# Performance work log

Measured on AMD Instinct MI355X. Metric: run time of the kernel, lower is better.

Reference implementation:

```python
import jax, jax.numpy as jnp
import numpy as np

N, M, D, H, T = 8192, 8192, 64, 32, 8
KERNEL_SCALE = 1.0


def setup_inputs() -> dict:
    key = jax.random.key(0)
    ks = jax.random.split(key, 8)
    s1 = 1.0 / np.sqrt(D)
    s2 = 1.0 / np.sqrt(H)
    return {
        "X": jax.random.normal(ks[0], (N, D), jnp.float32),
        "Y": jax.random.normal(ks[1], (M, D), jnp.float32),
        "Y_target": jax.random.normal(ks[2], (M, T), jnp.float32),
        "W1": jax.random.normal(ks[3], (D, H), jnp.float32) * s1,
        "b1": jnp.zeros((H,), jnp.float32),
        "W2": jax.random.normal(ks[4], (H, H), jnp.float32) * s2,
        "b2": jnp.zeros((H,), jnp.float32),
        "W3": jax.random.normal(ks[5], (H, H), jnp.float32) * s2,
        "b3": jnp.zeros((H,), jnp.float32),
    }


def _mlp(x, W1, b1, W2, b2, W3, b3):
    h = jax.nn.relu(x @ W1 + b1)
    h = jax.nn.relu(h @ W2 + b2)
    return jax.nn.relu(h @ W3 + b3)


def reference(X, Y, Y_target, W1, b1, W2, b2, W3, b3):
    Xf = _mlp(X, W1, b1, W2, b2, W3, b3)  # [N, H]
    Yf = _mlp(Y, W1, b1, W2, b2, W3, b3)  # [M, H]
    sq = (
        jnp.sum(Xf * Xf, axis=1, keepdims=True)
        + jnp.sum(Yf * Yf, axis=1)[None, :]
        - 2.0 * (Xf @ Yf.T)
    )
    sq = jnp.maximum(sq, 0.0)  # guard tiny negatives from cancellation
    kernel = jnp.exp(-sq / (2.0 * KERNEL_SCALE**2))  # [N, M]
    weights = kernel / jnp.sum(kernel, axis=1, keepdims=True)
    return weights @ Y_target  # [N, T]
```

## Files before the change

kernel.cpp:

```cpp
#include <hip/hip_runtime.h>
#include <hip/hip_bf16.h>
#include <cstddef>

#define N_ROWS 8192
#define M_ROWS 8192
#define D_IN   64
#define H_DIM  32
#define T_OUT  8
#define FDIM   48

#define NSPLIT   32
#define JSLICE   (M_ROWS / NSPLIT)
#define JTILE    32
#define NTILES   (JSLICE / JTILE)
#define LOG2E    1.4426950408889634f
#define NHALF_SC (-0.72134752044448169f)

#define KH_OFF 0
#define KL_OFF 3072
#define YH_OFF 6144
#define YL_OFF 8192
#define BUFSZ  10240
#define STAGESZ (2 * BUFSZ)

typedef _Float16 half8  __attribute__((ext_vector_type(8)));
typedef _Float16 half4v __attribute__((ext_vector_type(4)));
typedef __fp16   fp16x2 __attribute__((ext_vector_type(2)));
typedef float    f32x16 __attribute__((ext_vector_type(16)));

__device__ __forceinline__ half8 ld_h8(const _Float16* p) {
    return *(const half8*)p;
}


__global__ __launch_bounds__(256) void prep_kernel(
    const float* __restrict__ X, const float* __restrict__ Y,
    const float* __restrict__ Yt,
    const float* __restrict__ W1, const float* __restrict__ b1,
    const float* __restrict__ W2, const float* __restrict__ b2,
    const float* __restrict__ W3, const float* __restrict__ b3,
    _Float16* __restrict__ fh, _Float16* __restrict__ fl,
    _Float16* __restrict__ yfh, _Float16* __restrict__ yfl)
{
    __shared__ float xs [32 * 65];
    __shared__ float w1l[64 * 36];
    __shared__ float w2l[32 * 36];
    __shared__ float w3l[32 * 36];
    __shared__ float h1t[32 * 33];
    __shared__ float h2t[32 * 33];
    __shared__ float psums[8 * 32];
    __shared__ float bl[96];

    const int tid = threadIdx.x;

    if (blockIdx.x >= 512) {
        const int idx = (blockIdx.x - 512) * 256 + tid;
        const int lane = idx & 63;
        const int jtg  = idx >> 6;
        const int g    = jtg & 3;
        const int jt   = jtg >> 2;
        const int t    = lane & 31;
        const int h    = lane >> 5;
        const int j    = jt * 32 + g * 8 + h * 4;
        union { _Float16 hh[4]; uint2 u; } H, L;
        #pragma unroll
        for (int i = 0; i < 4; ++i) {
            float v = (t < T_OUT) ? Yt[(size_t)(j + i) * T_OUT + t]
                                  : (t == 8 ? 1.0f : 0.0f);
            _Float16 hi = (_Float16)v;
            H.hh[i] = hi;
            L.hh[i] = (_Float16)(v - (float)hi);
        }
        *(uint2*)(yfh + (size_t)idx * 4) = H.u;
        *(uint2*)(yfl + (size_t)idx * 4) = L.u;
        return;
    }

    const int rowbase = blockIdx.x * 32;
    const bool isX = rowbase < N_ROWS;
    const float* src = isX ? (X + (size_t)rowbase * D_IN)
                           : (Y + (size_t)(rowbase - N_ROWS) * D_IN);

    {
        const float4* g4 = (const float4*)src;
        int i0 = tid * 2;
        float4 v0 = g4[i0], v1 = g4[i0 + 1];
        int f0 = tid * 8;
        int r = f0 >> 6, c = f0 & 63;
        float* dst = xs + r * 65 + c;
        dst[0] = v0.x; dst[1] = v0.y; dst[2] = v0.z; dst[3] = v0.w;
        dst[4] = v1.x; dst[5] = v1.y; dst[6] = v1.z; dst[7] = v1.w;
    }
    {
        const float4* g4 = (const float4*)W1;
        int i0 = tid * 2;
        float4 v0 = g4[i0], v1 = g4[i0 + 1];
        int f0 = tid * 8;
        int r = f0 >> 5, c = f0 & 31;
        float* dst = w1l + r * 36 + c;
        ((float4*)dst)[0] = v0; ((float4*)dst)[1] = v1;
    }
    {
        int f0 = tid * 4;
        int r = f0 >> 5, c = f0 & 31;
        *(float4*)(w2l + r * 36 + c) = ((const float4*)W2)[tid];
        *(float4*)(w3l + r * 36 + c) = ((const float4*)W3)[tid];
    }
    if (tid < 32) { bl[tid] = b1[tid]; bl[32 + tid] = b2[tid]; bl[64 + tid] = b3[tid]; }
    __syncthreads();

    const int r  = tid & 31;
    const int c0 = (tid >> 5) * 4;

    float4 a1 = *(const float4*)(bl + c0);
    #pragma unroll
    for (int k = 0; k < 64; ++k) {
        float xv = xs[r * 65 + k];
        float4 w = *(const float4*)(w1l + k * 36 + c0);
        a1.x = fmaf(xv, w.x, a1.x);
        a1.y = fmaf(xv, w.y, a1.y);
        a1.z = fmaf(xv, w.z, a1.z);
        a1.w = fmaf(xv, w.w, a1.w);
    }
    h1t[(c0 + 0) * 33 + r] = fmaxf(a1.x, 0.f);
    h1t[(c0 + 1) * 33 + r] = fmaxf(a1.y, 0.f);
    h1t[(c0 + 2) * 33 + r] = fmaxf(a1.z, 0.f);
    h1t[(c0 + 3) * 33 + r] = fmaxf(a1.w, 0.f);
    __syncthreads();

    float4 a2 = *(const float4*)(bl + 32 + c0);
    #pragma unroll
    for (int k = 0; k < 32; ++k) {
        float xv = h1t[k * 33 + r];
        float4 w = *(const float4*)(w2l + k * 36 + c0);
        a2.x = fmaf(xv, w.x, a2.x);
        a2.y = fmaf(xv, w.y, a2.y);
        a2.z = fmaf(xv, w.z, a2.z);
        a2.w = fmaf(xv, w.w, a2.w);
    }
    h2t[(c0 + 0) * 33 + r] = fmaxf(a2.x, 0.f);
    h2t[(c0 + 1) * 33 + r] = fmaxf(a2.y, 0.f);
    h2t[(c0 + 2) * 33 + r] = fmaxf(a2.z, 0.f);
    h2t[(c0 + 3) * 33 + r] = fmaxf(a2.w, 0.f);
    __syncthreads();

    float4 a3 = *(const float4*)(bl + 64 + c0);
    #pragma unroll
    for (int k = 0; k < 32; ++k) {
        float xv = h2t[k * 33 + r];
        float4 w = *(const float4*)(w3l + k * 36 + c0);
        a3.x = fmaf(xv, w.x, a3.x);
        a3.y = fmaf(xv, w.y, a3.y);
        a3.z = fmaf(xv, w.z, a3.z);
        a3.w = fmaf(xv, w.w, a3.w);
    }
    float v0 = fmaxf(a3.x, 0.f), v1 = fmaxf(a3.y, 0.f);
    float v2 = fmaxf(a3.z, 0.f), v3 = fmaxf(a3.w, 0.f);

    psums[(tid >> 5) * 32 + r] = v0 * v0 + v1 * v1 + v2 * v2 + v3 * v3;

    const float scale = isX ? LOG2E : 1.0f;
    union { _Float16 h[4]; uint2 u; } hh, ll;
    float sv0 = v0 * scale, sv1 = v1 * scale, sv2 = v2 * scale, sv3 = v3 * scale;
    hh.h[0] = (_Float16)sv0; hh.h[1] = (_Float16)sv1;
    hh.h[2] = (_Float16)sv2; hh.h[3] = (_Float16)sv3;
    ll.h[0] = (_Float16)(sv0 - (float)hh.h[0]);
    ll.h[1] = (_Float16)(sv1 - (float)hh.h[1]);
    ll.h[2] = (_Float16)(sv2 - (float)hh.h[2]);
    ll.h[3] = (_Float16)(sv3 - (float)hh.h[3]);
    {
        const int tile = blockIdx.x;
        const int ch = c0 >> 4, hb = (c0 >> 3) & 1, off = c0 & 7;
        const size_t fi = (((size_t)(tile * 3 + ch) * 64) + hb * 32 + r) * 8 + off;
        *(uint2*)(fh + fi) = hh.u;
        *(uint2*)(fl + fi) = ll.u;
    }

    __syncthreads();
    if (tid < 32) {
        float nrm = 0.f;
        #pragma unroll
        for (int g = 0; g < 8; ++g) nrm += psums[g * 32 + tid];
        float qn = NHALF_SC * nrm;
        float d32 = isX ? qn : 1.0f;
        float d33 = isX ? 1.0f : qn;
        union { _Float16 h[8]; uint4 q; } eh, el, ez;
        #pragma unroll
        for (int i = 0; i < 8; ++i) { eh.h[i] = (_Float16)0.f; el.h[i] = (_Float16)0.f; ez.h[i] = (_Float16)0.f; }
        _Float16 h32 = (_Float16)d32, h33 = (_Float16)d33;
        eh.h[0] = h32; eh.h[1] = h33;
        el.h[0] = (_Float16)(d32 - (float)h32);
        el.h[1] = (_Float16)(d33 - (float)h33);
        const int tile = blockIdx.x;
        const size_t f0 = (((size_t)(tile * 3 + 2) * 64) + tid) * 8;
        const size_t f1 = (((size_t)(tile * 3 + 2) * 64) + 32 + tid) * 8;
        *(uint4*)(fh + f0) = eh.q;  *(uint4*)(fh + f1) = ez.q;
        *(uint4*)(fl + f0) = el.q;  *(uint4*)(fl + f1) = ez.q;
    }
}

__global__ __launch_bounds__(256, 4) void pair_kernel(
    const _Float16* __restrict__ fh, const _Float16* __restrict__ fl,
    const _Float16* __restrict__ yfh, const _Float16* __restrict__ yfl,
    float* __restrict__ pout, float* __restrict__ psum)
{
    __shared__ char smem[2 * STAGESZ];

    const int tid  = threadIdx.x;
    const int wave = tid >> 6;
    const int lane = tid & 63;
    const int n    = lane & 31;
    const int h    = lane >> 5;

    const int rowtile = blockIdx.x * 4 + wave;
    const int rowbase = rowtile * 32;
    const int s       = blockIdx.y;
    const int ktile0  = (N_ROWS / 32) + s * NTILES;

    const size_t qoff = (size_t)rowtile * 1536 + (size_t)lane * 8;
    half8 qh0 = ld_h8(fh + qoff);
    half8 qh1 = ld_h8(fh + qoff + 512);
    half8 qh2 = ld_h8(fh + qoff + 1024);
    half8 ql0 = ld_h8(fl + qoff);
    half8 ql1 = ld_h8(fl + qoff + 512);
    half8 ql2 = ld_h8(fl + qoff + 1024);

    auto prefetch = [&](int jt, char* buf) {
        const char* srcKh = (const char*)(fh + (size_t)(ktile0 + jt) * 1536);
        const char* srcKl = (const char*)(fl + (size_t)(ktile0 + jt) * 1536);
        const char* srcYh = (const char*)(yfh + (size_t)(s * NTILES + jt) * 1024);
        const char* srcYl = (const char*)(yfl + (size_t)(s * NTILES + jt) * 1024);
        #pragma unroll
        for (int r = 0; r < 3; ++r) {
            const int c0 = wave * 64 + r * 256;
            const int c  = c0 + lane;
            const char* g; char* l;
            if (c0 < 192)      { g = srcKh + (size_t)c * 16;         l = buf + KH_OFF + c * 16; }
            else if (c0 < 384) { g = srcKl + (size_t)(c - 192) * 16; l = buf + KL_OFF + (c - 192) * 16; }
            else if (c0 < 512) { g = srcYh + (size_t)(c - 384) * 16; l = buf + YH_OFF + (c - 384) * 16; }
            else if (c0 < 640) { g = srcYl + (size_t)(c - 512) * 16; l = buf + YL_OFF + (c - 512) * 16; }
            else break;
            __builtin_amdgcn_global_load_lds(
                (const __attribute__((address_space(1))) void*)g,
                (__attribute__((address_space(3))) void*)l, 16, 0, 0);
        }
    };

    f32x16 o = {};

    auto compute = [&](const char* cur) {
        half8 kh0 = *(const half8*)(cur + KH_OFF + lane * 16);
        half8 kh1 = *(const half8*)(cur + KH_OFF + 1024 + lane * 16);
        half8 kh2 = *(const half8*)(cur + KH_OFF + 2048 + lane * 16);
        half8 kl0 = *(const half8*)(cur + KL_OFF + lane * 16);
        half8 kl1 = *(const half8*)(cur + KL_OFF + 1024 + lane * 16);
        half8 kl2 = *(const half8*)(cur + KL_OFF + 2048 + lane * 16);

        f32x16 acc = {};
        acc = __builtin_amdgcn_mfma_f32_32x32x16_f16(kh0, qh0, acc, 0, 0, 0);
        acc = __builtin_amdgcn_mfma_f32_32x32x16_f16(kh1, qh1, acc, 0, 0, 0);
        acc = __builtin_amdgcn_mfma_f32_32x32x16_f16(kh2, qh2, acc, 0, 0, 0);
        acc = __builtin_amdgcn_mfma_f32_32x32x16_f16(kh0, ql0, acc, 0, 0, 0);
        acc = __builtin_amdgcn_mfma_f32_32x32x16_f16(kh1, ql1, acc, 0, 0, 0);
        acc = __builtin_amdgcn_mfma_f32_32x32x16_f16(kh2, ql2, acc, 0, 0, 0);
        acc = __builtin_amdgcn_mfma_f32_32x32x16_f16(kl0, qh0, acc, 0, 0, 0);
        acc = __builtin_amdgcn_mfma_f32_32x32x16_f16(kl1, qh1, acc, 0, 0, 0);
        acc = __builtin_amdgcn_mfma_f32_32x32x16_f16(kl2, qh2, acc, 0, 0, 0);

        half4v phi[4];
        #pragma unroll
        for (int g = 0; g < 4; ++g) {
            float w0 = __builtin_amdgcn_exp2f(fminf(acc[4*g+0], 0.f));
            float w1 = __builtin_amdgcn_exp2f(fminf(acc[4*g+1], 0.f));
            float w2 = __builtin_amdgcn_exp2f(fminf(acc[4*g+2], 0.f));
            float w3 = __builtin_amdgcn_exp2f(fminf(acc[4*g+3], 0.f));
            fp16x2 p01 = __builtin_amdgcn_cvt_pkrtz(w0, w1);
            fp16x2 p23 = __builtin_amdgcn_cvt_pkrtz(w2, w3);
            union { unsigned int u[2]; half4v v; } ph;
            ph.u[0] = __builtin_bit_cast(unsigned int, p01);
            ph.u[1] = __builtin_bit_cast(unsigned int, p23);
            phi[g] = ph.v;
        }

        #pragma unroll
        for (int g = 0; g < 4; ++g) {
            half4v bh = *(const half4v*)(cur + YH_OFF + (g * 64 + lane) * 8);
            half4v bv = *(const half4v*)(cur + YL_OFF + (g * 64 + lane) * 8);
            o = __builtin_amdgcn_mfma_f32_32x32x8f16(phi[g], bh, o, 0, 0, 0);
            o = __builtin_amdgcn_mfma_f32_32x32x8f16(phi[g], bv, o, 0, 0, 0);
        }
    };

    prefetch(0, smem);
    prefetch(1, smem + BUFSZ);
    __syncthreads();

    #pragma unroll
    for (int st = 0; st < NTILES / 2; ++st) {
        char* cur = smem + (st & 1) * STAGESZ;
        char* nxt = smem + ((st + 1) & 1) * STAGESZ;
        if (st + 1 < NTILES / 2) {
            prefetch(2 * st + 2, nxt);
            prefetch(2 * st + 3, nxt + BUFSZ);
        }
        compute(cur);
        compute(cur + BUFSZ);
        __syncthreads();
    }

    const int t = n;
    if (t <= 8) {
        #pragma unroll
        for (int r = 0; r < 16; ++r) {
            int i = (r & 3) + 8 * (r >> 2) + 4 * h;
            int row = rowbase + i;
            float v = o[r];
            if (t < 8)
                pout[((size_t)s * N_ROWS + row) * T_OUT + t] = v;
            else
                psum[(size_t)s * N_ROWS + row] = v;
        }
    }
}

__global__ __launch_bounds__(256) void reduce_kernel(
    const float* __restrict__ pout, const float* __restrict__ psum,
    float* __restrict__ out)
{
    const int id = blockIdx.x * 256 + threadIdx.x;
    const int i = id >> 3;
    float sv = 0.f, sw = 0.f;
    #pragma unroll
    for (int s = 0; s < NSPLIT; ++s) {
        sv += pout[(size_t)s * N_ROWS * T_OUT + id];
        sw += psum[(size_t)s * N_ROWS + i];
    }
    out[id] = sv / sw;
}

extern "C" void kernel_launch(void* const* d_in, const int* in_sizes, int n_in,
                              void* d_out, int out_size, void* d_ws, size_t ws_size,
                              hipStream_t stream)
{
    const float* X  = (const float*)d_in[0];
    const float* Y  = (const float*)d_in[1];
    const float* Yt = (const float*)d_in[2];
    const float* W1 = (const float*)d_in[3];
    const float* b1 = (const float*)d_in[4];
    const float* W2 = (const float*)d_in[5];
    const float* b2 = (const float*)d_in[6];
    const float* W3 = (const float*)d_in[7];
    const float* b3 = (const float*)d_in[8];
    float* out = (float*)d_out;

    char* ws = (char*)d_ws;
    const size_t n_feat = (size_t)((N_ROWS + M_ROWS) / 32) * 3 * 512;
    _Float16* fh  = (_Float16*)ws;   ws += n_feat * 2;
    _Float16* fl  = (_Float16*)ws;   ws += n_feat * 2;
    const size_t n_yf = (size_t)(M_ROWS / JTILE) * 4 * 64 * 4;
    _Float16* yfh = (_Float16*)ws;   ws += n_yf * 2;
    _Float16* yfl = (_Float16*)ws;   ws += n_yf * 2;
    float*    pout = (float*)ws;     ws += (size_t)NSPLIT * N_ROWS * T_OUT * 4;
    float*    psum = (float*)ws;

    prep_kernel<<<512 + 256, 256, 0, stream>>>(
        X, Y, Yt, W1, b1, W2, b2, W3, b3, fh, fl, yfh, yfl);

    dim3 grid2(N_ROWS / 128, NSPLIT);
    pair_kernel<<<grid2, 256, 0, stream>>>(fh, fl, yfh, yfl, pout, psum);

    reduce_kernel<<<(N_ROWS * T_OUT) / 256, 256, 0, stream>>>(pout, psum, out);
}
```

Baseline: 111.2 us.

## Interleave two key tiles per compute step and pack Y hi/lo together

The pair kernel now processes the two prefetched key tiles together, interleaving their MFMA chains into two independent accumulators (accA/accB, oA/oB). This hides MFMA dependency latency and gives the exp stage more independent work. The Y-target hi/lo halves are packed into one interleaved buffer, so a single 16-byte LDS load replaces two 8-byte loads. Launch bounds drop from 4 to 3 waves per SIMD to make room for the extra registers, which risks lower occupancy.

```diff
diff --git a/kernel.cpp b/kernel.cpp
--- a/kernel.cpp
+++ b/kernel.cpp
@@ -18,8 +18,7 @@
 
 #define KH_OFF 0
 #define KL_OFF 3072
-#define YH_OFF 6144
-#define YL_OFF 8192
+#define YI_OFF 6144
 #define BUFSZ  10240
 #define STAGESZ (2 * BUFSZ)
 
@@ -40,7 +39,7 @@
     const float* __restrict__ W2, const float* __restrict__ b2,
     const float* __restrict__ W3, const float* __restrict__ b3,
     _Float16* __restrict__ fh, _Float16* __restrict__ fl,
-    _Float16* __restrict__ yfh, _Float16* __restrict__ yfl)
+    _Float16* __restrict__ yfi)
 {
     __shared__ float xs [32 * 65];
     __shared__ float w1l[64 * 36];
@@ -62,17 +61,16 @@
         const int t    = lane & 31;
         const int h    = lane >> 5;
         const int j    = jt * 32 + g * 8 + h * 4;
-        union { _Float16 hh[4]; uint2 u; } H, L;
+        union { _Float16 hh[8]; uint4 u; } V;
         #pragma unroll
         for (int i = 0; i < 4; ++i) {
             float v = (t < T_OUT) ? Yt[(size_t)(j + i) * T_OUT + t]
                                   : (t == 8 ? 1.0f : 0.0f);
             _Float16 hi = (_Float16)v;
-            H.hh[i] = hi;
-            L.hh[i] = (_Float16)(v - (float)hi);
-        }
-        *(uint2*)(yfh + (size_t)idx * 4) = H.u;
-        *(uint2*)(yfl + (size_t)idx * 4) = L.u;
+            V.hh[i]     = hi;
+            V.hh[4 + i] = (_Float16)(v - (float)hi);
+        }
+        *(uint4*)(yfi + (size_t)idx * 8) = V.u;
         return;
     }
 
@@ -199,9 +197,9 @@
     }
 }
 
-__global__ __launch_bounds__(256, 4) void pair_kernel(
+__global__ __launch_bounds__(256, 3) void pair_kernel(
     const _Float16* __restrict__ fh, const _Float16* __restrict__ fl,
-    const _Float16* __restrict__ yfh, const _Float16* __restrict__ yfl,
+    const _Float16* __restrict__ yfi,
     float* __restrict__ pout, float* __restrict__ psum)
 {
     __shared__ char smem[2 * STAGESZ];
@@ -228,8 +226,7 @@
     auto prefetch = [&](int jt, char* buf) {
         const char* srcKh = (const char*)(fh + (size_t)(ktile0 + jt) * 1536);
         const char* srcKl = (const char*)(fl + (size_t)(ktile0 + jt) * 1536);
-        const char* srcYh = (const char*)(yfh + (size_t)(s * NTILES + jt) * 1024);
-        const char* srcYl = (const char*)(yfl + (size_t)(s * NTILES + jt) * 1024);
+        const char* srcYi = (const char*)(yfi + (size_t)(s * NTILES + jt) * 2048);
         #pragma unroll
         for (int r = 0; r < 3; ++r) {
             const int c0 = wave * 64 + r * 256;
@@ -237,8 +234,7 @@
             const char* g; char* l;
             if (c0 < 192)      { g = srcKh + (size_t)c * 16;         l = buf + KH_OFF + c * 16; }
             else if (c0 < 384) { g = srcKl + (size_t)(c - 192) * 16; l = buf + KL_OFF + (c - 192) * 16; }
-            else if (c0 < 512) { g = srcYh + (size_t)(c - 384) * 16; l = buf + YH_OFF + (c - 384) * 16; }
-            else if (c0 < 640) { g = srcYl + (size_t)(c - 512) * 16; l = buf + YL_OFF + (c - 512) * 16; }
+            else if (c0 < 640) { g = srcYi + (size_t)(c - 384) * 16; l = buf + YI_OFF + (c - 384) * 16; }
             else break;
             __builtin_amdgcn_global_load_lds(
                 (const __attribute__((address_space(1))) void*)g,
@@ -246,48 +242,72 @@
         }
     };
 
-    f32x16 o = {};
-
-    auto compute = [&](const char* cur) {
-        half8 kh0 = *(const half8*)(cur + KH_OFF + lane * 16);
-        half8 kh1 = *(const half8*)(cur + KH_OFF + 1024 + lane * 16);
-        half8 kh2 = *(const half8*)(cur + KH_OFF + 2048 + lane * 16);
-        half8 kl0 = *(const half8*)(cur + KL_OFF + lane * 16);
-        half8 kl1 = *(const half8*)(cur + KL_OFF + 1024 + lane * 16);
-        half8 kl2 = *(const half8*)(cur + KL_OFF + 2048 + lane * 16);
-
-        f32x16 acc = {};
-        acc = __builtin_amdgcn_mfma_f32_32x32x16_f16(kh0, qh0, acc, 0, 0, 0);
-        acc = __builtin_amdgcn_mfma_f32_32x32x16_f16(kh1, qh1, acc, 0, 0, 0);
-        acc = __builtin_amdgcn_mfma_f32_32x32x16_f16(kh2, qh2, acc, 0, 0, 0);
-        acc = __builtin_amdgcn_mfma_f32_32x32x16_f16(kh0, ql0, acc, 0, 0, 0);
-        acc = __builtin_amdgcn_mfma_f32_32x32x16_f16(kh1, ql1, acc, 0, 0, 0);
-        acc = __builtin_amdgcn_mfma_f32_32x32x16_f16(kh2, ql2, acc, 0, 0, 0);
-        acc = __builtin_amdgcn_mfma_f32_32x32x16_f16(kl0, qh0, acc, 0, 0, 0);
-        acc = __builtin_amdgcn_mfma_f32_32x32x16_f16(kl1, qh1, acc, 0, 0, 0);
-        acc = __builtin_amdgcn_mfma_f32_32x32x16_f16(kl2, qh2, acc, 0, 0, 0);
-
-        half4v phi[4];
+    f32x16 oA = {}, oB = {};
+
+    auto compute2 = [&](const char* A, const char* B) {
+        half8 akh0 = *(const half8*)(A + KH_OFF + lane * 16);
+        half8 bkh0 = *(const half8*)(B + KH_OFF + lane * 16);
+        half8 akh1 = *(const half8*)(A + KH_OFF + 1024 + lane * 16);
+        half8 bkh1 = *(const half8*)(B + KH_OFF + 1024 + lane * 16);
+        half8 akh2 = *(const half8*)(A + KH_OFF + 2048 + lane * 16);
+        half8 bkh2 = *(const half8*)(B + KH_OFF + 2048 + lane * 16);
+        half8 akl0 = *(const half8*)(A + KL_OFF + lane * 16);
+        half8 bkl0 = *(const half8*)(B + KL_OFF + lane * 16);
+        half8 akl1 = *(const half8*)(A + KL_OFF + 1024 + lane * 16);
+        half8 bkl1 = *(const half8*)(B + KL_OFF + 1024 + lane * 16);
+        half8 akl2 = *(const half8*)(A + KL_OFF + 2048 + lane * 16);
+        half8 bkl2 = *(const half8*)(B + KL_OFF + 2048 + lane * 16);
+
+        f32x16 accA = {}, accB = {};
+        accA = __builtin_amdgcn_mfma_f32_32x32x16_f16(akh0, qh0, accA, 0, 0, 0);
+        accB = __builtin_amdgcn_mfma_f32_32x32x16_f16(bkh0, qh0, accB, 0, 0, 0);
+        accA = __builtin_amdgcn_mfma_f32_32x32x16_f16(akh1, qh1, accA, 0, 0, 0);
+        accB = __builtin_amdgcn_mfma_f32_32x32x16_f16(bkh1, qh1, accB, 0, 0, 0);
+        accA = __builtin_amdgcn_mfma_f32_32x32x16_f16(akh2, qh2, accA, 0, 0, 0);
+        accB = __builtin_amdgcn_mfma_f32_32x32x16_f16(bkh2, qh2, accB, 0, 0, 0);
+        accA = __builtin_amdgcn_mfma_f32_32x32x16_f16(akh0, ql0, accA, 0, 0, 0);
+        accB = __builtin_amdgcn_mfma_f32_32x32x16_f16(bkh0, ql0, accB, 0, 0, 0);
+        accA = __builtin_amdgcn_mfma_f32_32x32x16_f16(akh1, ql1, accA, 0, 0, 0);
+        accB = __builtin_amdgcn_mfma_f32_32x32x16_f16(bkh1, ql1, accB, 0, 0, 0);
+        accA = __builtin_amdgcn_mfma_f32_32x32x16_f16(akh2, ql2, accA, 0, 0, 0);
+        accB = __builtin_amdgcn_mfma_f32_32x32x16_f16(bkh2, ql2, accB, 0, 0, 0);
+        accA = __builtin_amdgcn_mfma_f32_32x32x16_f16(akl0, qh0, accA, 0, 0, 0);
+        accB = __builtin_amdgcn_mfma_f32_32x32x16_f16(bkl0, qh0, accB, 0, 0, 0);
+        accA = __builtin_amdgcn_mfma_f32_32x32x16_f16(akl1, qh1, accA, 0, 0, 0);
+        accB = __builtin_amdgcn_mfma_f32_32x32x16_f16(bkl1, qh1, accB, 0, 0, 0);
+        accA = __builtin_amdgcn_mfma_f32_32x32x16_f16(akl2, qh2, accA, 0, 0, 0);
+        accB = __builtin_amdgcn_mfma_f32_32x32x16_f16(bkl2, qh2, accB, 0, 0, 0);
+
+        half4v phiA[4], phiB[4];
         #pragma unroll
         for (int g = 0; g < 4; ++g) {
-            float w0 = __builtin_amdgcn_exp2f(fminf(acc[4*g+0], 0.f));
-            float w1 = __builtin_amdgcn_exp2f(fminf(acc[4*g+1], 0.f));
-            float w2 = __builtin_amdgcn_exp2f(fminf(acc[4*g+2], 0.f));
-            float w3 = __builtin_amdgcn_exp2f(fminf(acc[4*g+3], 0.f));
-            fp16x2 p01 = __builtin_amdgcn_cvt_pkrtz(w0, w1);
-            fp16x2 p23 = __builtin_amdgcn_cvt_pkrtz(w2, w3);
-            union { unsigned int u[2]; half4v v; } ph;
-            ph.u[0] = __builtin_bit_cast(unsigned int, p01);
-            ph.u[1] = __builtin_bit_cast(unsigned int, p23);
-            phi[g] = ph.v;
+            float a0 = __builtin_amdgcn_exp2f(fminf(accA[4*g+0], 0.f));
+            float a1 = __builtin_amdgcn_exp2f(fminf(accA[4*g+1], 0.f));
+            float a2 = __builtin_amdgcn_exp2f(fminf(accA[4*g+2], 0.f));
+            float a3 = __builtin_amdgcn_exp2f(fminf(accA[4*g+3], 0.f));
+            float b0 = __builtin_amdgcn_exp2f(fminf(accB[4*g+0], 0.f));
+            float b1 = __builtin_amdgcn_exp2f(fminf(accB[4*g+1], 0.f));
+            float b2 = __builtin_amdgcn_exp2f(fminf(accB[4*g+2], 0.f));
+            float b3 = __builtin_amdgcn_exp2f(fminf(accB[4*g+3], 0.f));
+            union { unsigned int u[2]; half4v v; } pa, pb;
+            pa.u[0] = __builtin_bit_cast(unsigned int, __builtin_amdgcn_cvt_pkrtz(a0, a1));
+            pa.u[1] = __builtin_bit_cast(unsigned int, __builtin_amdgcn_cvt_pkrtz(a2, a3));
+            pb.u[0] = __builtin_bit_cast(unsigned int, __builtin_amdgcn_cvt_pkrtz(b0, b1));
+            pb.u[1] = __builtin_bit_cast(unsigned int, __builtin_amdgcn_cvt_pkrtz(b2, b3));
+            phiA[g] = pa.v; phiB[g] = pb.v;
         }
 
         #pragma unroll
         for (int g = 0; g < 4; ++g) {
-            half4v bh = *(const half4v*)(cur + YH_OFF + (g * 64 + lane) * 8);
-            half4v bv = *(const half4v*)(cur + YL_OFF + (g * 64 + lane) * 8);
-            o = __builtin_amdgcn_mfma_f32_32x32x8f16(phi[g], bh, o, 0, 0, 0);
-            o = __builtin_amdgcn_mfma_f32_32x32x8f16(phi[g], bv, o, 0, 0, 0);
+            uint4 ya = *(const uint4*)(A + YI_OFF + (g * 64 + lane) * 16);
+            uint4 yb = *(const uint4*)(B + YI_OFF + (g * 64 + lane) * 16);
+            union { unsigned int u[2]; half4v v; } ah, av, bh, bv;
+            ah.u[0] = ya.x; ah.u[1] = ya.y;  av.u[0] = ya.z; av.u[1] = ya.w;
+            bh.u[0] = yb.x; bh.u[1] = yb.y;  bv.u[0] = yb.z; bv.u[1] = yb.w;
+            oA = __builtin_amdgcn_mfma_f32_32x32x8f16(phiA[g], ah.v, oA, 0, 0, 0);
+            oB = __builtin_amdgcn_mfma_f32_32x32x8f16(phiB[g], bh.v, oB, 0, 0, 0);
+            oA = __builtin_amdgcn_mfma_f32_32x32x8f16(phiA[g], av.v, oA, 0, 0, 0);
+            oB = __builtin_amdgcn_mfma_f32_32x32x8f16(phiB[g], bv.v, oB, 0, 0, 0);
         }
     };
 
@@ -303,8 +323,7 @@
             prefetch(2 * st + 2, nxt);
             prefetch(2 * st + 3, nxt + BUFSZ);
         }
-        compute(cur);
-        compute(cur + BUFSZ);
+        compute2(cur, cur + BUFSZ);
         __syncthreads();
     }
 
@@ -314,7 +333,7 @@
         for (int r = 0; r < 16; ++r) {
             int i = (r & 3) + 8 * (r >> 2) + 4 * h;
             int row = rowbase + i;
-            float v = o[r];
+            float v = oA[r] + oB[r];
             if (t < 8)
                 pout[((size_t)s * N_ROWS + row) * T_OUT + t] = v;
             else
@@ -357,17 +376,16 @@
     const size_t n_feat = (size_t)((N_ROWS + M_ROWS) / 32) * 3 * 512;
     _Float16* fh  = (_Float16*)ws;   ws += n_feat * 2;
     _Float16* fl  = (_Float16*)ws;   ws += n_feat * 2;
-    const size_t n_yf = (size_t)(M_ROWS / JTILE) * 4 * 64 * 4;
-    _Float16* yfh = (_Float16*)ws;   ws += n_yf * 2;
-    _Float16* yfl = (_Float16*)ws;   ws += n_yf * 2;
+    const size_t n_yfi = (size_t)(M_ROWS / JTILE) * 4 * 64 * 8;
+    _Float16* yfi = (_Float16*)ws;   ws += n_yfi * 2;
     float*    pout = (float*)ws;     ws += (size_t)NSPLIT * N_ROWS * T_OUT * 4;
     float*    psum = (float*)ws;
 
     prep_kernel<<<512 + 256, 256, 0, stream>>>(
-        X, Y, Yt, W1, b1, W2, b2, W3, b3, fh, fl, yfh, yfl);
+        X, Y, Yt, W1, b1, W2, b2, W3, b3, fh, fl, yfi);
 
     dim3 grid2(N_ROWS / 128, NSPLIT);
-    pair_kernel<<<grid2, 256, 0, stream>>>(fh, fl, yfh, yfl, pout, psum);
+    pair_kernel<<<grid2, 256, 0, stream>>>(fh, fl, yfi, pout, psum);
 
     reduce_kernel<<<(N_ROWS * T_OUT) / 256, 256, 0, stream>>>(pout, psum, out);
 }
```

Measured after the change: 111.0 us. About the same (-0.1%).
